# Performance work log

Hardware: AMD Instinct MI355X
Metric: run time of the kernel (lower is better)

Reference implementation:

```python
import jax, jax.numpy as jnp
import numpy as np
import math

B, H, W, C = 8, 64, 64, 512
HEADS, DHEAD = 8, 64
LN_EPS = 1e-5


def layer_norm(x, g, b):
    mu = jnp.mean(x, axis=-1, keepdims=True)
    var = jnp.var(x, axis=-1, keepdims=True)
    return (x - mu) * jax.lax.rsqrt(var + LN_EPS) * g + b


def l2norm(x):
    n = jnp.sqrt(jnp.sum(x * x, axis=-1, keepdims=True))
    return x / jnp.maximum(n, 1e-12)


def dwconv3x3(x, w):
    # x: (B,C,H,W), w: (C,1,3,3) depthwise
    return jax.lax.conv_general_dilated(
        x, w, window_strides=(1, 1), padding='SAME',
        feature_group_count=x.shape[1],
        dimension_numbers=('NCHW', 'OIHW', 'NCHW'))


def setup_inputs() -> dict:
    key = jax.random.key(0)
    ks = jax.random.split(key, 16)
    s = 1.0 / math.sqrt(C)
    inp = {
        'x_in': jax.random.normal(ks[0], (B, H, W, C), jnp.float32),
        'illu_fea_trans': jax.random.normal(ks[1], (B, H, W, C), jnp.float32),
        'sem_fea_trans': jax.random.normal(ks[2], (B, H, W, C), jnp.float32),
        # SIF 1x1 convs as (C_in, C_out) matrices
        'Wk_sif': jax.random.normal(ks[3], (C, C), jnp.float32) * s,
        'Wq_sif': jax.random.normal(ks[4], (C, C), jnp.float32) * s,
        'Wv_sif': jax.random.normal(ks[5], (C, C), jnp.float32) * s,
        'ln_g': jnp.ones((C,), jnp.float32),
        'ln_b': jnp.zeros((C,), jnp.float32),
        # FG_MSA linears (in, out)
        'Wq': jax.random.normal(ks[6], (C, HEADS * DHEAD), jnp.float32) * s,
        'Wk': jax.random.normal(ks[7], (C, HEADS * DHEAD), jnp.float32) * s,
        'Wv': jax.random.normal(ks[8], (C, HEADS * DHEAD), jnp.float32) * s,
        'rescale': jnp.ones((HEADS, 1, 1), jnp.float32),
        'proj_w': jax.random.normal(ks[9], (HEADS * DHEAD, C), jnp.float32) * s,
        'proj_b': jnp.zeros((C,), jnp.float32),
        # depthwise conv pos-emb
        'dw1': jax.random.normal(ks[10], (C, 1, 3, 3), jnp.float32) * (1.0 / 3.0),
        'dw2': jax.random.normal(ks[11], (C, 1, 3, 3), jnp.float32) * (1.0 / 3.0),
    }
    return inp


def sif(illu, sem, Wk_sif, Wq_sif, Wv_sif, ln_g, ln_b):
    # illu, sem: (B, N, C); channel (C x C) cross-attention
    Kn = layer_norm(illu @ Wk_sif, ln_g, ln_b)          # (B,N,C)
    Qn = layer_norm(sem @ Wq_sif, ln_g, ln_b)           # (B,N,C)
    V = illu @ Wv_sif                                    # (B,N,C)
    Ab = jnp.einsum('bni,bnj->bij', Qn, Kn) / math.sqrt(C)  # (B,C,C)
    Ab = jax.nn.softmax(Ab, axis=-1)
    # (Ab @ V^T)^T + V ; SIF_FFN treated as identity (source not provided)
    return jnp.einsum('bij,bnj->bni', Ab, V) + V


def reference(x_in, illu_fea_trans, sem_fea_trans, Wk_sif, Wq_sif, Wv_sif,
              ln_g, ln_b, Wq, Wk, Wv, rescale, proj_w, proj_b, dw1, dw2):
    b, h, w, c = x_in.shape
    n = h * w
    x = x_in.reshape(b, n, c)
    q_inp = x @ Wq
    k_inp = x @ Wk
    v_inp = x @ Wv

    prior = sif(illu_fea_trans.reshape(b, n, c), sem_fea_trans.reshape(b, n, c),
                Wk_sif, Wq_sif, Wv_sif, ln_g, ln_b)      # (B,N,C)

    def split_heads(t):  # (b,n,h*d) -> (b,h,n,d)
        return t.reshape(b, n, HEADS, DHEAD).transpose(0, 2, 1, 3)

    q, k, v, g = map(split_heads, (q_inp, k_inp, v_inp, prior))
    v = v * g
    # transpose to (b,h,d,n), L2-normalize over n
    q = l2norm(q.transpose(0, 1, 3, 2))
    k = l2norm(k.transpose(0, 1, 3, 2))
    v = v.transpose(0, 1, 3, 2)
    attn = jnp.einsum('bhdn,bhen->bhde', k, q) * rescale  # (b,h,d,d)
    attn = jax.nn.softmax(attn, axis=-1)
    o = jnp.einsum('bhde,bhen->bhdn', attn, v)            # (b,h,d,n)
    o = o.transpose(0, 3, 1, 2).reshape(b, n, HEADS * DHEAD)
    out_c = (o @ proj_w + proj_b).reshape(b, h, w, c)

    vmap = v_inp.reshape(b, h, w, c).transpose(0, 3, 1, 2)  # NCHW
    p = dwconv3x3(vmap, dw1)
    p = jax.nn.gelu(p, approximate=False)
    p = dwconv3x3(p, dw2)
    out_p = p.transpose(0, 2, 3, 1)
    return out_c + out_p
```

## Files before the change

### kernel.cpp

```cpp
#include <hip/hip_runtime.h>

typedef unsigned short u16;
typedef unsigned int   u32;
typedef __bf16 bfx8 __attribute__((ext_vector_type(8)));
typedef float  f32x4 __attribute__((ext_vector_type(4)));

__device__ __forceinline__ float b2f(u16 v) {
    union { u32 u; float f; } c; c.u = ((u32)v) << 16; return c.f;
}
__device__ __forceinline__ u16 f2bf(float f) {
    union { float f; u32 u; } c; c.f = f;
    u32 u = c.u;
    return (u16)((u + 0x7fffu + ((u >> 16) & 1u)) >> 16);
}

__global__ void detect_dtype(const u16* __restrict__ x, int* __restrict__ flag)
{
    const int tid = threadIdx.x;
    int cnt = 0;
    for (int i = tid; i < 2048; i += 256) {
        const u16 v = x[2 * i];
        const int e = (v >> 7) & 0xFF;
        if ((v & 0x7fff) == 0 || (e >= 96 && e <= 144)) cnt++;
    }
#pragma unroll
    for (int off = 32; off > 0; off >>= 1) cnt += __shfl_xor(cnt, off);
    __shared__ int sred[4];
    if ((tid & 63) == 0) sred[tid >> 6] = cnt;
    __syncthreads();
    if (tid == 0) {
        const int total = sred[0] + sred[1] + sred[2] + sred[3];
        flag[0] = (total < 1024) ? 1 : 0;
    }
}

__global__ void to_bf16(const void* __restrict__ in, u16* __restrict__ out,
                        int n, const int* __restrict__ flag)
{
    const int i = blockIdx.x * 256 + threadIdx.x;
    if (i < n)
        out[i] = (*flag) ? f2bf(((const float*)in)[i]) : ((const u16*)in)[i];
}

__global__ __launch_bounds__(256, 2)
void gemm_bt(const void* __restrict__ A, const u16* __restrict__ Bt,
             void* __restrict__ C,
             int M, int N, int K, int lda, int ldb, int ldc,
             long sAb, long sAh, long sBb, long sBh, long sCb, long sCh, int nh,
             int epi_mode, const u16* __restrict__ add1, long sAddB, long sAddH,
             int ldadd, const u16* __restrict__ mul1, const u16* __restrict__ bias,
             const int* __restrict__ aF32, const int* __restrict__ cF32)
{
    __shared__ __align__(16) u16 As[128 * 40];
    __shared__ __align__(16) u16 Bs[128 * 40];
    const bool af32 = aF32 && (*aF32 != 0);
    const bool cf32 = cF32 && (*cF32 != 0);
    const int z = blockIdx.z, zb = z / nh, zh = z - zb * nh;
    const long aoff = (long)zb * sAb + (long)zh * sAh;
    Bt += (long)zb * sBb + (long)zh * sBh;
    const long coff = (long)zb * sCb + (long)zh * sCh;
    const int m0 = blockIdx.x * 128, n0 = blockIdx.y * 128;
    const int tid = threadIdx.x, lane = tid & 63, wave = tid >> 6;
    const int wm = (wave >> 1) * 64, wn = (wave & 1) * 64;
    const int q = lane >> 4, l16 = lane & 15;
    const int rowL = tid >> 2, kcol = (tid & 3) * 8;

    f32x4 acc[4][4] = {};

    for (int k0 = 0; k0 < K; k0 += 32) {
#pragma unroll
        for (int p = 0; p < 2; ++p) {
            const int r = rowL + p * 64;
            uint4 va = {0, 0, 0, 0}, vb = {0, 0, 0, 0};
            if (m0 + r < M) {
                const long ai = aoff + (long)(m0 + r) * lda + k0 + kcol;
                if (af32) {
                    const float* Af = (const float*)A + ai;
                    float4 f0 = *(const float4*)Af;
                    float4 f1 = *(const float4*)(Af + 4);
                    u16* u = (u16*)&va;
                    u[0] = f2bf(f0.x); u[1] = f2bf(f0.y);
                    u[2] = f2bf(f0.z); u[3] = f2bf(f0.w);
                    u[4] = f2bf(f1.x); u[5] = f2bf(f1.y);
                    u[6] = f2bf(f1.z); u[7] = f2bf(f1.w);
                } else {
                    va = *(const uint4*)((const u16*)A + ai);
                }
            }
            if (n0 + r < N) vb = *(const uint4*)(Bt + (long)(n0 + r) * ldb + k0 + kcol);
            *(uint4*)(&As[r * 40 + kcol]) = va;
            *(uint4*)(&Bs[r * 40 + kcol]) = vb;
        }
        __syncthreads();
        bfx8 af[4], bfr[4];
#pragma unroll
        for (int t = 0; t < 4; ++t) {
            af[t]  = *(const bfx8*)(&As[(wm + t * 16 + l16) * 40 + q * 8]);
            bfr[t] = *(const bfx8*)(&Bs[(wn + t * 16 + l16) * 40 + q * 8]);
        }
#pragma unroll
        for (int i = 0; i < 4; ++i)
#pragma unroll
            for (int j = 0; j < 4; ++j)
                acc[i][j] = __builtin_amdgcn_mfma_f32_16x16x32_bf16(af[i], bfr[j], acc[i][j], 0, 0, 0);
        __syncthreads();
    }

#pragma unroll
    for (int i = 0; i < 4; ++i) {
#pragma unroll
        for (int j = 0; j < 4; ++j) {
#pragma unroll
            for (int r = 0; r < 4; ++r) {
                const int gm = m0 + wm + i * 16 + q * 4 + r;
                const int gn = n0 + wn + j * 16 + l16;
                if (gm < M && gn < N) {
                    float v = acc[i][j][r];
                    const long cidx = coff + (long)gm * ldc + gn;
                    if (epi_mode == 2) {
                        const long aidx = (long)zb * sAddB + (long)zh * sAddH + (long)gm * ldadd + gn;
                        v = (v + b2f(add1[aidx])) * b2f(mul1[aidx]);
                    } else if (epi_mode == 3) {
                        const long aidx = (long)gm * ldadd + gn;
                        v = v + b2f(bias[gn]) + b2f(add1[aidx]);
                    }
                    if (cf32) ((float*)C)[cidx] = v;
                    else      ((u16*)C)[cidx] = f2bf(v);
                }
            }
        }
    }
}

__global__ __launch_bounds__(256, 2)
void gemm_at(const u16* __restrict__ A, const u16* __restrict__ B,
             float* __restrict__ C,
             int M, int N, int K, int lda, int ldb, int ldc,
             long sAb, long sAh, long sBb, long sBh, long sCb, long sCh, int nh)
{
    __shared__ __align__(16) u16 At[128 * 64];
    __shared__ __align__(16) u16 Bl[128 * 64];
    const int z = blockIdx.z, zb = z / nh, zh = z - zb * nh;
    A += (long)zb * sAb + (long)zh * sAh;
    B += (long)zb * sBb + (long)zh * sBh;
    const long coff = (long)zb * sCb + (long)zh * sCh;
    const int i0 = blockIdx.x * 128, j0 = blockIdx.y * 128;
    const int tid = threadIdx.x, lane = tid & 63, wave = tid >> 6;
    const int wm = (wave >> 1) * 64, wn = (wave & 1) * 64;
    const int q = lane >> 4, l16 = lane & 15;
    const int tr = tid >> 4, tc8 = (tid & 15) * 8;
    const int sw = (tc8 >> 3) & 7;

    f32x4 acc[4][4] = {};

    for (int n0 = 0; n0 < K; n0 += 64) {
#pragma unroll
        for (int p = 0; p < 4; ++p) {
            const int nn = tr + p * 16;
            uint4 va = {0, 0, 0, 0}, vb = {0, 0, 0, 0};
            if (i0 + tc8 < M) va = *(const uint4*)(A + (long)(n0 + nn) * lda + i0 + tc8);
            if (j0 + tc8 < N) vb = *(const uint4*)(B + (long)(n0 + nn) * ldb + j0 + tc8);
            const u16* ua = (const u16*)&va;
            const u16* ub = (const u16*)&vb;
#pragma unroll
            for (int e = 0; e < 8; ++e) {
                const int k = nn ^ ((e ^ sw) << 3);
                At[(tc8 + e) * 64 + k] = ua[e];
                Bl[(tc8 + e) * 64 + k] = ub[e];
            }
        }
        __syncthreads();
#pragma unroll
        for (int ks = 0; ks < 2; ++ks) {
            bfx8 af[4], bfr[4];
#pragma unroll
            for (int t = 0; t < 4; ++t) {
                const int ra = wm + t * 16 + l16;
                const int sa = ((ra & 7) ^ ((ra >> 3) & 7)) << 3;
                af[t]  = *(const bfx8*)(&At[ra * 64 + ((ks * 32 + q * 8) ^ sa)]);
                const int rb = wn + t * 16 + l16;
                const int sb = ((rb & 7) ^ ((rb >> 3) & 7)) << 3;
                bfr[t] = *(const bfx8*)(&Bl[rb * 64 + ((ks * 32 + q * 8) ^ sb)]);
            }
#pragma unroll
            for (int i = 0; i < 4; ++i)
#pragma unroll
                for (int j = 0; j < 4; ++j)
                    acc[i][j] = __builtin_amdgcn_mfma_f32_16x16x32_bf16(af[i], bfr[j], acc[i][j], 0, 0, 0);
        }
        __syncthreads();
    }

#pragma unroll
    for (int i = 0; i < 4; ++i)
#pragma unroll
        for (int j = 0; j < 4; ++j)
#pragma unroll
            for (int r = 0; r < 4; ++r) {
                const int gm = i0 + wm + i * 16 + q * 4 + r;
                const int gn = j0 + wn + j * 16 + l16;
                if (gm < M && gn < N)
                    C[coff + (long)gm * ldc + gn] = acc[i][j][r];
            }
}

__global__ void transpose_k(const void* __restrict__ in, u16* __restrict__ out,
                            const int* __restrict__ dflag)
{
    __shared__ __align__(16) u16 tile[64 * 72];
    const bool f32 = (*dflag != 0);
    const int r0 = blockIdx.x * 64, c0 = blockIdx.y * 64;
    const int tid = threadIdx.x;
    {
        const int tr = tid >> 3, tc = (tid & 7) * 8;
#pragma unroll
        for (int p = 0; p < 2; ++p) {
            const int r = tr + p * 32;
            const long base = (long)(r0 + r) * 512 + c0 + tc;
#pragma unroll
            for (int e = 0; e < 8; ++e) {
                tile[r * 72 + tc + e] = f32 ? f2bf(((const float*)in)[base + e])
                                            : ((const u16*)in)[base + e];
            }
        }
    }
    __syncthreads();
    {
        const int oc = tid >> 3, rn = (tid & 7) * 8;
#pragma unroll
        for (int p = 0; p < 2; ++p) {
            const int c = oc + p * 32;
            u16 res[8];
#pragma unroll
            for (int i = 0; i < 8; ++i) res[i] = tile[(rn + i) * 72 + c];
            *(uint4*)(out + (long)(c0 + c) * 512 + r0 + rn) = *(uint4*)res;
        }
    }
}

__global__ void ln_stats(const u16* __restrict__ in, float* __restrict__ mu,
                         float* __restrict__ rstd)
{
    const long row = blockIdx.x;
    const u16* p = in + row * 512;
    const int tid = threadIdx.x;
    const float v0 = b2f(p[tid * 2]), v1 = b2f(p[tid * 2 + 1]);
    float s = v0 + v1, sq = v0 * v0 + v1 * v1;
#pragma unroll
    for (int off = 32; off > 0; off >>= 1) {
        s  += __shfl_xor(s, off);
        sq += __shfl_xor(sq, off);
    }
    __shared__ float ls[4], lq[4];
    if ((tid & 63) == 0) { ls[tid >> 6] = s; lq[tid >> 6] = sq; }
    __syncthreads();
    if (tid == 0) {
        s = ls[0] + ls[1] + ls[2] + ls[3];
        sq = lq[0] + lq[1] + lq[2] + lq[3];
        const float m = s * (1.0f / 512.0f);
        float var = sq * (1.0f / 512.0f) - m * m;
        var = fmaxf(var, 0.0f);
        mu[row] = m;
        rstd[row] = rsqrtf(var + 1e-5f);
    }
}

__global__ void ln_apply(u16* __restrict__ x, const float* __restrict__ mu,
                         const float* __restrict__ rstd,
                         const u16* __restrict__ g, const u16* __restrict__ b)
{
    const long idx = (long)blockIdx.x * 256 + threadIdx.x;
    const long row = idx >> 6;
    const int  c8  = (int)(idx & 63) * 8;
    u16* p = x + row * 512 + c8;
    uint4 v = *(uint4*)p;
    u16* u = (u16*)&v;
    const float m_ = mu[row], rs = rstd[row];
#pragma unroll
    for (int i = 0; i < 8; ++i)
        u[i] = f2bf((b2f(u[i]) - m_) * rs * b2f(g[c8 + i]) + b2f(b[c8 + i]));
    *(uint4*)p = v;
}

__global__ void zero_f32(float* __restrict__ p, int n)
{
    const int i = blockIdx.x * 256 + threadIdx.x;
    if (i < n) p[i] = 0.0f;
}

__global__ void colssq(const u16* __restrict__ in, float* __restrict__ ssq, int rowsPerChunk)
{
    const int b = blockIdx.x, cchunk = blockIdx.y, nchunk = blockIdx.z;
    const int c = cchunk * 256 + threadIdx.x;
    const u16* p = in + (long)b * 4096 * 512 + (long)nchunk * rowsPerChunk * 512 + c;
    float acc = 0.f;
    for (int n = 0; n < rowsPerChunk; ++n) {
        const float v = b2f(p[(long)n * 512]);
        acc += v * v;
    }
    atomicAdd(&ssq[b * 512 + c], acc);
}

__global__ void softmax_ab(const float* __restrict__ Ab, u16* __restrict__ out,
                           long sstride, int nsplit)
{
    const long row = blockIdx.x;
    const float* p = Ab + row * 512;
    const int tid = threadIdx.x;
    const float scale = 0.044194173824159216f;
    float a = 0.f, b = 0.f;
    for (int s = 0; s < nsplit; ++s) {
        a += p[(long)s * sstride + tid];
        b += p[(long)s * sstride + tid + 256];
    }
    a *= scale; b *= scale;
    float m = fmaxf(a, b);
#pragma unroll
    for (int off = 32; off > 0; off >>= 1) m = fmaxf(m, __shfl_xor(m, off));
    __shared__ float red[8];
    if ((tid & 63) == 0) red[tid >> 6] = m;
    __syncthreads();
    m = fmaxf(fmaxf(red[0], red[1]), fmaxf(red[2], red[3]));
    const float e0 = __expf(a - m), e1 = __expf(b - m);
    float s = e0 + e1;
#pragma unroll
    for (int off = 32; off > 0; off >>= 1) s += __shfl_xor(s, off);
    if ((tid & 63) == 0) red[4 + (tid >> 6)] = s;
    __syncthreads();
    s = red[4] + red[5] + red[6] + red[7];
    const float inv = 1.0f / fmaxf(s, 1e-30f);
    out[row * 512 + tid]       = f2bf(e0 * inv);
    out[row * 512 + tid + 256] = f2bf(e1 * inv);
}

__global__ void softmax_g(const float* __restrict__ G, const u16* __restrict__ rescale,
                          const float* __restrict__ ssq_k, const float* __restrict__ ssq_q,
                          u16* __restrict__ out, long sstride, int nsplit)
{
    const int row = blockIdx.x * 4 + (threadIdx.x >> 6);
    const int lane = threadIdx.x & 63;
    const int zz = row >> 6, d = row & 63;
    const int b_ = zz >> 3, h = zz & 7;
    const float rk = 1.0f / fmaxf(sqrtf(fmaxf(ssq_k[b_ * 512 + h * 64 + d], 0.f)), 1e-12f);
    const float rq = 1.0f / fmaxf(sqrtf(fmaxf(ssq_q[b_ * 512 + h * 64 + lane], 0.f)), 1e-12f);
    float gv = 0.f;
    for (int s = 0; s < nsplit; ++s)
        gv += G[(long)s * sstride + (long)row * 64 + lane];
    const float v = gv * rk * rq * b2f(rescale[h]);
    float m = v;
#pragma unroll
    for (int off = 32; off > 0; off >>= 1) m = fmaxf(m, __shfl_xor(m, off));
    const float e = __expf(v - m);
    float s = e;
#pragma unroll
    for (int off = 32; off > 0; off >>= 1) s += __shfl_xor(s, off);
    out[(long)row * 64 + lane] = f2bf(e / fmaxf(s, 1e-30f));
}

__global__ void dwconv3x3(const u16* __restrict__ in, const u16* __restrict__ w,
                          u16* __restrict__ out, int do_gelu)
{
    __shared__ u16 wl[4608];
    const int tid = threadIdx.x;
    for (int i = tid; i < 4608; i += 256) wl[i] = w[i];
    __syncthreads();
    const int b = blockIdx.x >> 6, y = blockIdx.x & 63;
    const long base = (long)b * 64 * 64 * 512;
    for (int t = 0; t < 16; ++t) {
        const int idx = t * 256 + tid;
        const int cg = idx & 63, x = idx >> 6;
        float acc[8] = {};
#pragma unroll
        for (int dy = -1; dy <= 1; ++dy) {
            const int yy = y + dy;
            if (yy < 0 || yy > 63) continue;
#pragma unroll
            for (int dx = -1; dx <= 1; ++dx) {
                const int xx = x + dx;
                if (xx < 0 || xx > 63) continue;
                const uint4 v = *(const uint4*)(in + base + ((long)yy * 64 + xx) * 512 + cg * 8);
                const u16* u = (const u16*)&v;
                const int wo = (dy + 1) * 3 + (dx + 1);
#pragma unroll
                for (int i = 0; i < 8; ++i)
                    acc[i] += b2f(u[i]) * b2f(wl[(cg * 8 + i) * 9 + wo]);
            }
        }
        u16 res[8];
#pragma unroll
        for (int i = 0; i < 8; ++i) {
            float v = acc[i];
            if (do_gelu) v = 0.5f * v * (1.0f + erff(v * 0.70710678118654752f));
            res[i] = f2bf(v);
        }
        *(uint4*)(out + base + ((long)y * 64 + x) * 512 + cg * 8) = *(uint4*)res;
    }
}

extern "C" void kernel_launch(void* const* d_in, const int* in_sizes, int n_in,
                              void* d_out, int out_size, void* d_ws, size_t ws_size,
                              hipStream_t stream)
{
    const void* x     = d_in[0];
    const void* illu  = d_in[1];
    const void* sem   = d_in[2];
    const void* WkS   = d_in[3];
    const void* WqS   = d_in[4];
    const void* WvS   = d_in[5];
    const void* ln_g  = d_in[6];
    const void* ln_b  = d_in[7];
    const void* Wq    = d_in[8];
    const void* Wk    = d_in[9];
    const void* Wv    = d_in[10];
    const void* resc  = d_in[11];
    const void* projW = d_in[12];
    const void* projB = d_in[13];
    const void* dw1   = d_in[14];
    const void* dw2   = d_in[15];
    (void)in_sizes; (void)n_in; (void)out_size; (void)ws_size;

    char* ws = (char*)d_ws;
    size_t off = 0;
    auto nxt = [&](size_t bytes) -> void* {
        void* p = ws + off;
        off += (bytes + 255) & ~(size_t)255;
        return p;
    };

    u16* WqT   = (u16*)nxt(524288);
    u16* WkT   = (u16*)nxt(524288);
    u16* WvT   = (u16*)nxt(524288);
    u16* WkST  = (u16*)nxt(524288);
    u16* WqST  = (u16*)nxt(524288);
    u16* WvST  = (u16*)nxt(524288);
    u16* projT = (u16*)nxt(524288);
    u16* A = (u16*)nxt(33554432);
    u16* B = (u16*)nxt(33554432);
    u16* C = (u16*)nxt(33554432);
    float* Abf  = (float*)nxt(8388608);
    u16*   Absm = (u16*)nxt(4194304);
    float* mu   = (float*)nxt(131072);
    float* rs   = (float*)nxt(131072);
    float* ssq_q = (float*)nxt(16384);
    float* ssq_k = (float*)nxt(16384);
    float* Gf   = (float*)nxt(1048576);
    u16*   attn = (u16*)nxt(524288);
    int*   dflag = (int*)nxt(256);
    u16* ln_gc  = (u16*)nxt(1024);
    u16* ln_bc  = (u16*)nxt(1024);
    u16* projBc = (u16*)nxt(1024);
    u16* rescc  = (u16*)nxt(256);
    u16* dw1c   = (u16*)nxt(9216);
    u16* dw2c   = (u16*)nxt(9216);
    (void)Gf;

    const dim3 blk(256);

    detect_dtype<<<dim3(1), blk, 0, stream>>>((const u16*)x, dflag);
    to_bf16<<<dim3(2), blk, 0, stream>>>(ln_g,  ln_gc,  512,  dflag);
    to_bf16<<<dim3(2), blk, 0, stream>>>(ln_b,  ln_bc,  512,  dflag);
    to_bf16<<<dim3(2), blk, 0, stream>>>(projB, projBc, 512,  dflag);
    to_bf16<<<dim3(1), blk, 0, stream>>>(resc,  rescc,  8,    dflag);
    to_bf16<<<dim3(18), blk, 0, stream>>>(dw1,  dw1c,   4608, dflag);
    to_bf16<<<dim3(18), blk, 0, stream>>>(dw2,  dw2c,   4608, dflag);

    auto wT = [&](const void* w, u16* o) {
        transpose_k<<<dim3(8, 8, 1), blk, 0, stream>>>(w, o, dflag);
    };
    wT(Wq, WqT); wT(Wk, WkT); wT(Wv, WvT);
    wT(WkS, WkST); wT(WqS, WqST); wT(WvS, WvST); wT(projW, projT);

    auto gemm = [&](const void* Ap, const u16* Btp, void* Cp, int M, int N, int K,
                    int lda, int ldb, int ldc, int nz, int nh,
                    long sAb, long sAh, long sBb, long sBh, long sCb, long sCh,
                    int epi, const u16* add1, long sAddB, long sAddH, int ldadd,
                    const u16* mul1, const u16* bias,
                    const int* aF32, const int* cF32) {
        dim3 g((M + 127) / 128, (N + 127) / 128, nz);
        gemm_bt<<<g, blk, 0, stream>>>(Ap, Btp, Cp, M, N, K, lda, ldb, ldc,
            sAb, sAh, sBb, sBh, sCb, sCh, nh, epi, add1, sAddB, sAddH, ldadd,
            mul1, bias, aF32, cF32);
    };

    gemm(illu, WkST, A, 32768, 512, 512, 512, 512, 512, 1, 1, 0,0,0,0,0,0, 1,
         nullptr,0,0,0, nullptr, nullptr, dflag, nullptr);
    ln_stats<<<dim3(32768), blk, 0, stream>>>(A, mu, rs);
    ln_apply<<<dim3(8192), blk, 0, stream>>>(A, mu, rs, ln_gc, ln_bc);
    gemm(sem, WqST, B, 32768, 512, 512, 512, 512, 512, 1, 1, 0,0,0,0,0,0, 1,
         nullptr,0,0,0, nullptr, nullptr, dflag, nullptr);
    ln_stats<<<dim3(32768), blk, 0, stream>>>(B, mu, rs);
    ln_apply<<<dim3(8192), blk, 0, stream>>>(B, mu, rs, ln_gc, ln_bc);
    float* Cf = (float*)C;
    gemm_at<<<dim3(4, 4, 16), blk, 0, stream>>>(B, A, Cf, 512, 512, 2048,
        512, 512, 512, 1048576, 2097152, 1048576, 2097152, 2097152, 262144, 8);
    softmax_ab<<<dim3(4096), blk, 0, stream>>>(Cf, Absm, 2097152, 2);

    gemm(x, WqT, A, 32768, 512, 512, 512, 512, 512, 1, 1, 0,0,0,0,0,0, 1,
         nullptr,0,0,0, nullptr, nullptr, dflag, nullptr);
    zero_f32<<<dim3(16), blk, 0, stream>>>(ssq_q, 4096);
    colssq<<<dim3(8, 2, 16), blk, 0, stream>>>(A, ssq_q, 256);
    gemm(x, WkT, B, 32768, 512, 512, 512, 512, 512, 1, 1, 0,0,0,0,0,0, 1,
         nullptr,0,0,0, nullptr, nullptr, dflag, nullptr);
    zero_f32<<<dim3(16), blk, 0, stream>>>(ssq_k, 4096);
    colssq<<<dim3(8, 2, 16), blk, 0, stream>>>(B, ssq_k, 256);
    gemm_at<<<dim3(1, 1, 256), blk, 0, stream>>>(B, A, Abf, 64, 64, 1024,
        512, 512, 64, 524288, 64, 524288, 64, 262144, 4096, 64);
    softmax_g<<<dim3(1024), blk, 0, stream>>>(Abf, rescc, ssq_k, ssq_q, attn,
        262144, 4);

    gemm(x, WvT, A, 32768, 512, 512, 512, 512, 512, 1, 1, 0,0,0,0,0,0, 1,
         nullptr,0,0,0, nullptr, nullptr, dflag, nullptr);
    gemm(illu, WvST, B, 32768, 512, 512, 512, 512, 512, 1, 1, 0,0,0,0,0,0, 1,
         nullptr,0,0,0, nullptr, nullptr, dflag, nullptr);
    gemm(B, Absm, C, 4096, 512, 512, 512, 512, 512, 8, 1,
         2097152, 0, 262144, 0, 2097152, 0, 2, B, 2097152, 0, 512, A, nullptr,
         nullptr, nullptr);
    gemm(C, attn, B, 4096, 64, 64, 512, 64, 512, 64, 8,
         2097152, 64, 32768, 4096, 2097152, 64, 1, nullptr,0,0,0, nullptr, nullptr,
         nullptr, nullptr);
    dwconv3x3<<<dim3(512), blk, 0, stream>>>(A, dw1c, C, 1);
    dwconv3x3<<<dim3(512), blk, 0, stream>>>(C, dw2c, A, 0);
    gemm(B, projT, d_out, 32768, 512, 512, 512, 512, 512, 1, 1, 0,0,0,0,0,0,
         3, A, 0, 0, 512, nullptr, projBc, nullptr, dflag);
}
```

Baseline: 1.109 ms.

## Swizzle GEMM blocks across XCDs, split-K reductions wider, pre-convert x to bf16

Adds an XCD-aware block index remap to both GEMM kernels so that neighbouring tiles land on the same chiplet's L2. The split-K count of the two channel-attention reductions is doubled, giving more workgroups with shorter K loops, and the softmax kernels now sum the extra partials. x is converted to bf16 once with a vectorized kernel and reused by the three projection GEMMs instead of each GEMM converting fp32 on load. In-GEMM fp32-to-bf16 conversion switches to the hardware cast. This costs an extra conversion pass and more partial-sum traffic.

```diff
diff --git a/kernel.cpp b/kernel.cpp
--- a/kernel.cpp
+++ b/kernel.cpp
@@ -12,6 +12,26 @@
     union { float f; u32 u; } c; c.f = f;
     u32 u = c.u;
     return (u16)((u + 0x7fffu + ((u >> 16) & 1u)) >> 16);
+}
+__device__ __forceinline__ u16 f2bf_hw(float f) {
+    __bf16 h = (__bf16)f;
+    return *(u16*)&h;
+}
+
+__device__ __forceinline__ void xcd_swz(int& bx, int& by, int& bz)
+{
+    const int gx = gridDim.x, gy = gridDim.y, gz = gridDim.z;
+    const int nwg = gx * gy * gz;
+    const int flat = blockIdx.x + gx * (blockIdx.y + gy * blockIdx.z);
+    int w = flat;
+    if ((nwg & 7) == 0) {
+        const int q = nwg >> 3;
+        w = (flat & 7) * q + (flat >> 3);
+    }
+    by = w % gy;
+    const int t = w / gy;
+    bx = t % gx;
+    bz = t / gx;
 }
 
 __global__ void detect_dtype(const u16* __restrict__ x, int* __restrict__ flag)
@@ -40,6 +60,26 @@
     const int i = blockIdx.x * 256 + threadIdx.x;
     if (i < n)
         out[i] = (*flag) ? f2bf(((const float*)in)[i]) : ((const u16*)in)[i];
+}
+
+__global__ void to_bf16_v8(const void* __restrict__ in, u16* __restrict__ out,
+                           int n8, const int* __restrict__ flag)
+{
+    const int i = blockIdx.x * 256 + threadIdx.x;
+    if (i >= n8) return;
+    uint4 r;
+    if (*flag) {
+        const float4 f0 = ((const float4*)in)[2 * i];
+        const float4 f1 = ((const float4*)in)[2 * i + 1];
+        u16* u = (u16*)&r;
+        u[0] = f2bf_hw(f0.x); u[1] = f2bf_hw(f0.y);
+        u[2] = f2bf_hw(f0.z); u[3] = f2bf_hw(f0.w);
+        u[4] = f2bf_hw(f1.x); u[5] = f2bf_hw(f1.y);
+        u[6] = f2bf_hw(f1.z); u[7] = f2bf_hw(f1.w);
+    } else {
+        r = ((const uint4*)in)[i];
+    }
+    ((uint4*)out)[i] = r;
 }
 
 __global__ __launch_bounds__(256, 2)
@@ -55,11 +95,13 @@
     __shared__ __align__(16) u16 Bs[128 * 40];
     const bool af32 = aF32 && (*aF32 != 0);
     const bool cf32 = cF32 && (*cF32 != 0);
-    const int z = blockIdx.z, zb = z / nh, zh = z - zb * nh;
+    int bx, by, bz;
+    xcd_swz(bx, by, bz);
+    const int z = bz, zb = z / nh, zh = z - zb * nh;
     const long aoff = (long)zb * sAb + (long)zh * sAh;
     Bt += (long)zb * sBb + (long)zh * sBh;
     const long coff = (long)zb * sCb + (long)zh * sCh;
-    const int m0 = blockIdx.x * 128, n0 = blockIdx.y * 128;
+    const int m0 = bx * 128, n0 = by * 128;
     const int tid = threadIdx.x, lane = tid & 63, wave = tid >> 6;
     const int wm = (wave >> 1) * 64, wn = (wave & 1) * 64;
     const int q = lane >> 4, l16 = lane & 15;
@@ -79,10 +121,10 @@
                     float4 f0 = *(const float4*)Af;
                     float4 f1 = *(const float4*)(Af + 4);
                     u16* u = (u16*)&va;
-                    u[0] = f2bf(f0.x); u[1] = f2bf(f0.y);
-                    u[2] = f2bf(f0.z); u[3] = f2bf(f0.w);
-                    u[4] = f2bf(f1.x); u[5] = f2bf(f1.y);
-                    u[6] = f2bf(f1.z); u[7] = f2bf(f1.w);
+                    u[0] = f2bf_hw(f0.x); u[1] = f2bf_hw(f0.y);
+                    u[2] = f2bf_hw(f0.z); u[3] = f2bf_hw(f0.w);
+                    u[4] = f2bf_hw(f1.x); u[5] = f2bf_hw(f1.y);
+                    u[6] = f2bf_hw(f1.z); u[7] = f2bf_hw(f1.w);
                 } else {
                     va = *(const uint4*)((const u16*)A + ai);
                 }
@@ -140,11 +182,13 @@
 {
     __shared__ __align__(16) u16 At[128 * 64];
     __shared__ __align__(16) u16 Bl[128 * 64];
-    const int z = blockIdx.z, zb = z / nh, zh = z - zb * nh;
+    int bx, by, bz;
+    xcd_swz(bx, by, bz);
+    const int z = bz, zb = z / nh, zh = z - zb * nh;
     A += (long)zb * sAb + (long)zh * sAh;
     B += (long)zb * sBb + (long)zh * sBh;
     const long coff = (long)zb * sCb + (long)zh * sCh;
-    const int i0 = blockIdx.x * 128, j0 = blockIdx.y * 128;
+    const int i0 = bx * 128, j0 = by * 128;
     const int tid = threadIdx.x, lane = tid & 63, wave = tid >> 6;
     const int wm = (wave >> 1) * 64, wn = (wave & 1) * 64;
     const int q = lane >> 4, l16 = lane & 15;
@@ -491,25 +535,27 @@
     ln_stats<<<dim3(32768), blk, 0, stream>>>(B, mu, rs);
     ln_apply<<<dim3(8192), blk, 0, stream>>>(B, mu, rs, ln_gc, ln_bc);
     float* Cf = (float*)C;
-    gemm_at<<<dim3(4, 4, 16), blk, 0, stream>>>(B, A, Cf, 512, 512, 2048,
-        512, 512, 512, 1048576, 2097152, 1048576, 2097152, 2097152, 262144, 8);
-    softmax_ab<<<dim3(4096), blk, 0, stream>>>(Cf, Absm, 2097152, 2);
-
-    gemm(x, WqT, A, 32768, 512, 512, 512, 512, 512, 1, 1, 0,0,0,0,0,0, 1,
-         nullptr,0,0,0, nullptr, nullptr, dflag, nullptr);
+    gemm_at<<<dim3(4, 4, 32), blk, 0, stream>>>(B, A, Cf, 512, 512, 1024,
+        512, 512, 512, 524288, 2097152, 524288, 2097152, 2097152, 262144, 8);
+    softmax_ab<<<dim3(4096), blk, 0, stream>>>(Cf, Absm, 2097152, 4);
+
+    u16* xb = C;
+    to_bf16_v8<<<dim3(8192), blk, 0, stream>>>(x, xb, 2097152, dflag);
+    gemm(xb, WqT, A, 32768, 512, 512, 512, 512, 512, 1, 1, 0,0,0,0,0,0, 1,
+         nullptr,0,0,0, nullptr, nullptr, nullptr, nullptr);
     zero_f32<<<dim3(16), blk, 0, stream>>>(ssq_q, 4096);
     colssq<<<dim3(8, 2, 16), blk, 0, stream>>>(A, ssq_q, 256);
-    gemm(x, WkT, B, 32768, 512, 512, 512, 512, 512, 1, 1, 0,0,0,0,0,0, 1,
-         nullptr,0,0,0, nullptr, nullptr, dflag, nullptr);
+    gemm(xb, WkT, B, 32768, 512, 512, 512, 512, 512, 1, 1, 0,0,0,0,0,0, 1,
+         nullptr,0,0,0, nullptr, nullptr, nullptr, nullptr);
     zero_f32<<<dim3(16), blk, 0, stream>>>(ssq_k, 4096);
     colssq<<<dim3(8, 2, 16), blk, 0, stream>>>(B, ssq_k, 256);
-    gemm_at<<<dim3(1, 1, 256), blk, 0, stream>>>(B, A, Abf, 64, 64, 1024,
-        512, 512, 64, 524288, 64, 524288, 64, 262144, 4096, 64);
+    gemm_at<<<dim3(1, 1, 512), blk, 0, stream>>>(B, A, Abf, 64, 64, 512,
+        512, 512, 64, 262144, 64, 262144, 64, 262144, 4096, 64);
     softmax_g<<<dim3(1024), blk, 0, stream>>>(Abf, rescc, ssq_k, ssq_q, attn,
-        262144, 4);
-
-    gemm(x, WvT, A, 32768, 512, 512, 512, 512, 512, 1, 1, 0,0,0,0,0,0, 1,
-         nullptr,0,0,0, nullptr, nullptr, dflag, nullptr);
+        262144, 8);
+
+    gemm(xb, WvT, A, 32768, 512, 512, 512, 512, 512, 1, 1, 0,0,0,0,0,0, 1,
+         nullptr,0,0,0, nullptr, nullptr, nullptr, nullptr);
     gemm(illu, WvST, B, 32768, 512, 512, 512, 512, 512, 1, 1, 0,0,0,0,0,0, 1,
          nullptr,0,0,0, nullptr, nullptr, dflag, nullptr);
     gemm(B, Absm, C, 4096, 512, 512, 512, 512, 512, 8, 1,
```

Result: faster. 1.040 ms (-6.2%).
